# Kernel optimization log

Measured on AMD Instinct MI355X. Metric: run time of the kernel, lower is better.

## Reference

```python
import jax, jax.numpy as jnp
import numpy as np

B, S, WP = 64, 128, 18          # batch, words/sentence, padded chars/word
K = 3                            # char window size (module constant)
E = 128                          # embedding_dim
H = 256                          # hidden_dim
L = 4                            # cnn out channels (l=4 in module)
V = 50000                        # vocab size
A = 100                          # alphabet size
T = 50                           # tagset size


def setup_inputs() -> dict:
    key = jax.random.key(0)
    ks = jax.random.split(key, 14)
    n = lambda k, *sh: jax.random.normal(k, sh, dtype=jnp.float32) * 0.1
    return {
        "char_ids": jax.random.randint(ks[0], (B, S, WP), 0, A),
        "word_ids": jax.random.randint(ks[1], (B, S), 0, V),
        "char_emb": n(ks[2], A, E),
        "word_emb": n(ks[3], V + 1, E),
        "cnn_w": n(ks[4], L, K * E),
        "cnn_b": n(ks[5], L),
        "wih_f": n(ks[6], 4 * H, E),
        "whh_f": n(ks[7], 4 * H, H),
        "b_f": n(ks[8], 4 * H),
        "wih_b": n(ks[9], 4 * H, E),
        "whh_b": n(ks[10], 4 * H, H),
        "b_b": n(ks[11], 4 * H),
        "out_w": n(ks[12], T, 2 * H),
        "out_b": n(ks[13], T),
    }


def _lstm(x, Wih, Whh, b, reverse):
    # x: [S, B, E] -> hs: [S, B, H]; PyTorch gate order i, f, g, o
    hdim = Whh.shape[1]

    def step(carry, xt):
        h, c = carry
        z = xt @ Wih.T + h @ Whh.T + b
        i, f, g, o = jnp.split(z, 4, axis=-1)
        c = jax.nn.sigmoid(f) * c + jax.nn.sigmoid(i) * jnp.tanh(g)
        h = jax.nn.sigmoid(o) * jnp.tanh(c)
        return (h, c), h

    h0 = jnp.zeros((x.shape[1], hdim), x.dtype)
    _, hs = jax.lax.scan(step, (h0, h0), x, reverse=reverse)
    return hs


def reference(char_ids, word_ids, char_emb, word_emb, cnn_w, cnn_b,
              wih_f, whh_f, b_f, wih_b, whh_b, b_b, out_w, out_b):
    # --- per-word char CNN + max-pool (fully batched over B, S, positions) ---
    ce = char_emb[char_ids]                        # [B, S, WP, E]
    W = WP - (K - 1)                               # window positions per word
    windows = jnp.concatenate([ce[:, :, i:i + W] for i in range(K)], axis=-1)  # [B,S,W,K*E]
    phi = jnp.einsum('bswd,cd->bswc', windows, cnn_w) + cnn_b                  # [B,S,W,L]
    char_reprs = phi.max(axis=2)                   # [B, S, L] (unused by tag path, as in original)

    # --- word embeddings -> BiLSTM -> linear -> log_softmax over seq dim ---
    we = word_emb[word_ids]                        # [B, S, E]
    x = we.transpose(1, 0, 2)                      # [S, B, E]
    hf = _lstm(x, wih_f, whh_f, b_f, reverse=False)
    hb = _lstm(x, wih_b, whh_b, b_b, reverse=True)
    lstm_out = jnp.concatenate([hf, hb], axis=-1).transpose(1, 0, 2)  # [B, S, 2H]
    tag_space = lstm_out @ out_w.T + out_b         # [B, S, T]
    tag_scores = jax.nn.log_softmax(tag_space, axis=1)  # dim=1 as in original
    return tag_scores, char_reprs
```

## Files before the change

### kernel.cpp

```cpp
#include <hip/hip_runtime.h>
#include <hip/hip_bf16.h>

#define B_  64
#define S_  128
#define WP_ 18
#define K_  3
#define E_  128
#define H_  256
#define L_  4
#define T_  50

typedef __hip_bfloat16 bf16;

__device__ __forceinline__ float b2f(bf16 x) { return __bfloat162float(x); }
__device__ __forceinline__ bf16  f2b(float x) { return __float2bfloat16(x); }

__device__ __forceinline__ float fast_sigmoid(float x) {
    return 1.f / (1.f + __expf(-x));
}
__device__ __forceinline__ float fast_tanh(float x) {
    float a = fminf(fmaxf(2.f * x, -30.f), 30.f);
    float e = __expf(a);
    return (e - 1.f) / (e + 1.f);
}
__device__ __forceinline__ unsigned int pack2(float lo, float hi) {
    bf16 l = f2b(lo), h = f2b(hi);
    unsigned short ls = *(unsigned short*)&l, hs = *(unsigned short*)&h;
    return ((unsigned int)hs << 16) | ls;
}

#define DOT2(z, w, h) asm("v_dot2_f32_bf16 %0, %1, %2, %0" : "+v"(z) : "v"(w), "v"(h))
#define PIN4(V_) asm volatile("" : "+v"((V_).x), "+v"((V_).y), "+v"((V_).z), "+v"((V_).w))

__global__ void k_prep(const float* __restrict__ whh_f, const float* __restrict__ whh_b,
                       const float* __restrict__ wih_f, const float* __restrict__ wih_b,
                       unsigned int* __restrict__ wp_f, unsigned int* __restrict__ wp_b,
                       unsigned int* __restrict__ wihT2_f, unsigned int* __restrict__ wihT2_b) {
    int blk = blockIdx.x, t = threadIdx.x;
    if (blk < 1024) {
        const float* src   = (blk < 512) ? whh_f : whh_b;
        unsigned int* dst  = (blk < 512) ? wp_f  : wp_b;
        int d = ((blk & 511) << 8) + t;
        int m = d >> 12, rem = d & 4095;
        int td = rem >> 2, epair = rem & 3, e = epair << 1;
        int i = td >> 2, p = td & 3, g = m >> 3, kk = m & 7;
        int col = (g << 8) + i;
        int k = (p << 6) + (kk << 3) + e;
        float2 sv = *(const float2*)(src + col * 256 + k);
        dst[d] = pack2(sv.x, sv.y);
    } else {
        int id = blk - 1024;
        const float* src  = (id < 256) ? wih_f   : wih_b;
        unsigned int* dst = (id < 256) ? wihT2_f : wihT2_b;
        int d = ((id & 255) << 8) + t;
        int kp = d >> 10, j = d & 1023;
        float2 sv = *(const float2*)(src + j * 128 + 2 * kp);
        dst[d] = pack2(sv.x, sv.y);
    }
}

__global__ void k_input_proj(const int* __restrict__ word_ids,
                             const float* __restrict__ word_emb,
                             const unsigned int* __restrict__ wihT2_f, const float* __restrict__ b_f,
                             const unsigned int* __restrict__ wihT2_b, const float* __restrict__ b_b,
                             bf16* __restrict__ igq_f, bf16* __restrict__ igq_b) {
    int dir = blockIdx.y;
    const unsigned int* wihT2 = dir ? wihT2_b : wihT2_f;
    const float* bb  = dir ? b_b   : b_f;
    bf16* igq        = dir ? igq_b : igq_f;
    __shared__ unsigned int x2[32][64];
    int t  = threadIdx.x;
    int r0 = blockIdx.x * 32;
    for (int u = t; u < 32 * 64; u += 512) {
        int rr = u >> 6, ep = u & 63;
        int r = r0 + rr;
        int s = r >> 6, b = r & 63;
        int wid = word_ids[b * S_ + s];
        float2 ev = *(const float2*)(word_emb + (size_t)wid * E_ + 2 * ep);
        x2[rr][ep] = pack2(ev.x, ev.y);
    }
    __syncthreads();
    int j = t & 255, jh = t >> 8;
    float acc[2][32];
    #pragma unroll
    for (int c2 = 0; c2 < 2; ++c2) {
        float bv = bb[j + (2 * jh + c2) * 256];
        #pragma unroll
        for (int rr = 0; rr < 32; ++rr) acc[c2][rr] = bv;
    }
    for (int kp = 0; kp < 64; ++kp) {
        unsigned int wv0 = wihT2[kp * 1024 + j + (2 * jh) * 256];
        unsigned int wv1 = wihT2[kp * 1024 + j + (2 * jh + 1) * 256];
        #pragma unroll
        for (int rr = 0; rr < 32; ++rr) {
            unsigned int xp = x2[rr][kp];
            DOT2(acc[0][rr], wv0, xp);
            DOT2(acc[1][rr], wv1, xp);
        }
    }
    #pragma unroll
    for (int rr = 0; rr < 32; ++rr)
        *(unsigned int*)(igq + (size_t)(r0 + rr) * 1024 + j * 4 + 2 * jh) =
            pack2(acc[0][rr], acc[1][rr]);
}

__global__ __launch_bounds__(1024, 4) void k_lstm_cnn(
        const bf16* __restrict__ igq_f, const bf16* __restrict__ igq_b,
        const uint4* __restrict__ wp_f, const uint4* __restrict__ wp_b,
        unsigned int* __restrict__ hfp, unsigned int* __restrict__ hbp,
        const int* __restrict__ char_ids, const float* __restrict__ char_emb,
        const float* __restrict__ cnn_w, const float* __restrict__ cnn_b,
        float* __restrict__ out_char) {
    __shared__ uint4 wlds[9216];
    __shared__ __align__(16) unsigned int hpbuf[2][160];

    int t = threadIdx.x;

    if (blockIdx.x < 128) {
        int b   = blockIdx.x & 63;
        int dir = blockIdx.x >> 6;
        const bf16* igq  = dir ? igq_b : igq_f;
        const uint4* wp  = dir ? wp_b  : wp_f;
        unsigned int* hs = dir ? hbp   : hfp;

        int i = t >> 2, p = t & 3;

        for (int u = t; u < 9216; u += 1024) wlds[u] = wp[23 * 1024 + u];
        if (t < 320) ((unsigned int*)hpbuf)[t] = 0;
        float c_reg = 0.f;

        uint4 wreg[23];
        #pragma unroll
        for (int m = 0; m < 23; ++m) {
            wreg[m] = wp[m * 1024 + t];
            PIN4(wreg[m]);
        }
        __syncthreads();

        int cur = 0;
        int s0 = dir ? (S_ - 1) : 0;
        uint2 igu = *(const uint2*)&igq[((size_t)s0 * B_ + b) * 1024 + i * 4];

        for (int step = 0; step < S_; ++step) {
            int s = dir ? (S_ - 1 - step) : step;

            float z0 = 0.f, z1 = 0.f, z2 = 0.f, z3 = 0.f;
            if (p == 0) {
                z0 = __uint_as_float(igu.x << 16);
                z1 = __uint_as_float(igu.x & 0xffff0000u);
                z2 = __uint_as_float(igu.y << 16);
                z3 = __uint_as_float(igu.y & 0xffff0000u);
            }
            const char* hpc = (const char*)hpbuf[cur];
            #pragma unroll
            for (int kk = 0; kk < 8; ++kk) {
                uint4 hv = *(const uint4*)(hpc + p * 144 + kk * 16);
                {   uint4 wv = wreg[kk];
                    DOT2(z0, wv.x, hv.x); DOT2(z0, wv.y, hv.y);
                    DOT2(z0, wv.z, hv.z); DOT2(z0, wv.w, hv.w); }
                {   uint4 wv = wreg[8 + kk];
                    DOT2(z1, wv.x, hv.x); DOT2(z1, wv.y, hv.y);
                    DOT2(z1, wv.z, hv.z); DOT2(z1, wv.w, hv.w); }
                {   uint4 wv = (kk < 7) ? wreg[16 + kk] : wlds[t];
                    DOT2(z2, wv.x, hv.x); DOT2(z2, wv.y, hv.y);
                    DOT2(z2, wv.z, hv.z); DOT2(z2, wv.w, hv.w); }
                {   uint4 wv = wlds[(1 + kk) * 1024 + t];
                    DOT2(z3, wv.x, hv.x); DOT2(z3, wv.y, hv.y);
                    DOT2(z3, wv.z, hv.z); DOT2(z3, wv.w, hv.w); }
            }
            if (step + 1 < S_) {
                int sn = dir ? (S_ - 2 - step) : (step + 1);
                igu = *(const uint2*)&igq[((size_t)sn * B_ + b) * 1024 + i * 4];
            }
            z0 += __shfl_xor(z0, 1); z0 += __shfl_xor(z0, 2);
            z1 += __shfl_xor(z1, 1); z1 += __shfl_xor(z1, 2);
            z2 += __shfl_xor(z2, 1); z2 += __shfl_xor(z2, 2);
            z3 += __shfl_xor(z3, 1); z3 += __shfl_xor(z3, 2);
            if (p == 0) {
                float si = fast_sigmoid(z0);
                float sf = fast_sigmoid(z1);
                float tg = fast_tanh(z2);
                float so = fast_sigmoid(z3);
                c_reg = sf * c_reg + si * tg;
                float hn = so * fast_tanh(c_reg);
                char* dstb = (char*)hpbuf[cur ^ 1] + (i >> 6) * 144 + ((i >> 1) & 31) * 4 + (i & 1) * 2;
                *(bf16*)dstb = f2b(hn);
            }
            __syncthreads();
            if (t < 128) {
                hs[((size_t)s * B_ + b) * 128 + t] =
                    hpbuf[cur ^ 1][(t >> 5) * 36 + (t & 31)];
            }
            cur ^= 1;
        }
    } else {
        unsigned int* pool_u = (unsigned int*)wlds;
        float*        pool_f = (float*)wlds;
        int blkc = blockIdx.x - 128;

        for (int u = t; u < 4 * 192; u += 1024) {
            int c = u / 192, pe = u % 192;
            pool_u[c * 196 + pe] = pack2(cnn_w[c * 384 + 2 * pe], cnn_w[c * 384 + 2 * pe + 1]);
        }
        if (t < 4) pool_f[784 + t] = cnn_b[t];
        __syncthreads();

        int wv = t >> 6, lane = t & 63;
        unsigned int* cew = pool_u + 800 + wv * 1224;
        int pos = lane >> 2, c = lane & 3;

        #pragma unroll 1
        for (int j = 0; j < 4; ++j) {
            int word = (blkc * 16 + wv) * 4 + j;
            const int* ids = char_ids + word * WP_;
            for (int row = 0; row < WP_; ++row) {
                float2 ev = *(const float2*)(char_emb + (size_t)ids[row] * 128 + 2 * lane);
                cew[row * 68 + lane] = pack2(ev.x, ev.y);
            }
            float acc = 0.f;
            #pragma unroll
            for (int i = 0; i < K_; ++i) {
                const uint4* cr = (const uint4*)(cew + (pos + i) * 68);
                const uint4* wr = (const uint4*)(pool_u + c * 196 + i * 64);
                #pragma unroll
                for (int q = 0; q < 16; ++q) {
                    uint4 cv = cr[q], wq = wr[q];
                    DOT2(acc, wq.x, cv.x); DOT2(acc, wq.y, cv.y);
                    DOT2(acc, wq.z, cv.z); DOT2(acc, wq.w, cv.w);
                }
            }
            acc += pool_f[784 + c];
            #pragma unroll
            for (int off = 4; off < 64; off <<= 1) acc = fmaxf(acc, __shfl_xor(acc, off));
            if (lane < L_) out_char[(size_t)word * L_ + lane] = acc;
        }
    }
}

__global__ __launch_bounds__(1024) void k_tag_linear(
        const unsigned int* __restrict__ hfp, const unsigned int* __restrict__ hbp,
        const float* __restrict__ out_w, const float* __restrict__ out_b,
        float* __restrict__ tag) {
    __shared__ unsigned int ow[50 * 257];
    __shared__ unsigned int hv[16][256];
    int bs0 = blockIdx.x * 16;
    int t = threadIdx.x;
    for (int u = t; u < 12800; u += 1024) {
        int tt = u >> 8, kp = u & 255;
        float2 wv = *(const float2*)(out_w + tt * 512 + 2 * kp);
        ow[tt * 257 + kp] = pack2(wv.x, wv.y);
    }
    for (int u = t; u < 16 * 256; u += 1024) {
        int w = u >> 8, q = u & 255;
        int bs = bs0 + w;
        int b = bs >> 7, s = bs & 127;
        const unsigned int* src = (q < 128) ? hfp : hbp;
        hv[w][q] = src[((size_t)s * B_ + b) * 128 + (q & 127)];
    }
    __syncthreads();
    int w = t >> 6, tt = t & 63;
    if (tt < T_) {
        int bs = bs0 + w;
        int b = bs >> 7, s = bs & 127;
        float acc = out_b[tt];
        const unsigned int* owr = &ow[tt * 257];
        const unsigned int* hvr = hv[w];
        #pragma unroll 8
        for (int kp = 0; kp < 256; ++kp) DOT2(acc, owr[kp], hvr[kp]);
        tag[((size_t)b * T_ + tt) * S_ + s] = acc;
    }
}

__global__ void k_log_softmax(const float* __restrict__ tag, float* __restrict__ out) {
    int wid  = (blockIdx.x * 256 + threadIdx.x) >> 6;
    int lane = threadIdx.x & 63;
    if (wid >= B_ * T_) return;
    int b = wid / T_, t = wid % T_;
    const float* row = tag + (size_t)wid * S_;
    float v0 = row[lane], v1 = row[lane + 64];
    float m = fmaxf(v0, v1);
    #pragma unroll
    for (int off = 32; off; off >>= 1) m = fmaxf(m, __shfl_xor(m, off));
    float e = expf(v0 - m) + expf(v1 - m);
    #pragma unroll
    for (int off = 32; off; off >>= 1) e += __shfl_xor(e, off);
    float lse = m + logf(e);
    out[((size_t)b * S_ + lane)      * T_ + t] = v0 - lse;
    out[((size_t)b * S_ + lane + 64) * T_ + t] = v1 - lse;
}

extern "C" void kernel_launch(void* const* d_in, const int* in_sizes, int n_in,
                              void* d_out, int out_size, void* d_ws, size_t ws_size,
                              hipStream_t stream) {
    const int*   char_ids = (const int*)d_in[0];
    const int*   word_ids = (const int*)d_in[1];
    const float* char_emb = (const float*)d_in[2];
    const float* word_emb = (const float*)d_in[3];
    const float* cnn_w    = (const float*)d_in[4];
    const float* cnn_b    = (const float*)d_in[5];
    const float* wih_f    = (const float*)d_in[6];
    const float* whh_f    = (const float*)d_in[7];
    const float* b_f      = (const float*)d_in[8];
    const float* wih_b    = (const float*)d_in[9];
    const float* whh_b    = (const float*)d_in[10];
    const float* b_b      = (const float*)d_in[11];
    const float* out_w    = (const float*)d_in[12];
    const float* out_b    = (const float*)d_in[13];
    float* out = (float*)d_out;
    char* ws   = (char*)d_ws;

    size_t o = 0;
    unsigned int* wihT2_f = (unsigned int*)(ws + o); o += (size_t)64 * 1024 * 4;
    unsigned int* wihT2_b = (unsigned int*)(ws + o); o += (size_t)64 * 1024 * 4;
    unsigned int* wp_f    = (unsigned int*)(ws + o); o += (size_t)1024 * 128 * 4;
    unsigned int* wp_b    = (unsigned int*)(ws + o); o += (size_t)1024 * 128 * 4;
    bf16* igq_f  = (bf16*)(ws + o); o += (size_t)S_ * B_ * 1024 * 2;
    bf16* igq_b  = (bf16*)(ws + o); o += (size_t)S_ * B_ * 1024 * 2;
    unsigned int* hfp = (unsigned int*)(ws + o); o += (size_t)S_ * B_ * 128 * 4;
    unsigned int* hbp = (unsigned int*)(ws + o); o += (size_t)S_ * B_ * 128 * 4;
    float* tag   = (float*)(ws + o); o += (size_t)B_ * T_ * S_ * 4;

    k_prep<<<1536, 256, 0, stream>>>(whh_f, whh_b, wih_f, wih_b,
                                     wp_f, wp_b, wihT2_f, wihT2_b);
    k_input_proj<<<dim3(256, 2), 512, 0, stream>>>(word_ids, word_emb,
                                                   wihT2_f, b_f, wihT2_b, b_b, igq_f, igq_b);
    k_lstm_cnn<<<256, 1024, 0, stream>>>(igq_f, igq_b,
                                         (const uint4*)wp_f, (const uint4*)wp_b, hfp, hbp,
                                         char_ids, char_emb, cnn_w, cnn_b,
                                         out + (size_t)B_ * S_ * T_);
    k_tag_linear<<<B_ * S_ / 16, 1024, 0, stream>>>(hfp, hbp, out_w, out_b, tag);
    k_log_softmax<<<(B_ * T_ + 3) / 4, 256, 0, stream>>>(tag, out);
}
```

Measured before the change: 374.0 us.

## Halve LSTM block to 512 threads, two threads per hidden unit, more weights in registers

The recurrent LSTM block now uses 512 threads, each hidden unit split across 2 threads instead of 4. Each thread keeps 56 uint4 weight vectors in registers and reads only 8 from LDS. The weight packing in prep and the CNN word partition are reworked to match. The goal is to move more Whh reads from LDS into registers and shorten the cross-lane reduction, so each sequential step has less latency. In exchange each thread does twice the dot products and register pressure becomes very high, which risks spills.

```diff
diff --git a/kernel.cpp b/kernel.cpp
--- a/kernel.cpp
+++ b/kernel.cpp
@@ -41,11 +41,12 @@
         const float* src   = (blk < 512) ? whh_f : whh_b;
         unsigned int* dst  = (blk < 512) ? wp_f  : wp_b;
         int d = ((blk & 511) << 8) + t;
-        int m = d >> 12, rem = d & 4095;
-        int td = rem >> 2, epair = rem & 3, e = epair << 1;
-        int i = td >> 2, p = td & 3, g = m >> 3, kk = m & 7;
+        int m2 = d >> 11, rem = d & 2047;
+        int u = rem >> 2, e2 = rem & 3;
+        int i = u >> 1, p2 = u & 1;
+        int g = m2 >> 4, kk2 = m2 & 15;
         int col = (g << 8) + i;
-        int k = (p << 6) + (kk << 3) + e;
+        int k = (p2 << 7) + (kk2 << 3) + (e2 << 1);
         float2 sv = *(const float2*)(src + col * 256 + k);
         dst[d] = pack2(sv.x, sv.y);
     } else {
@@ -104,7 +105,7 @@
             pack2(acc[0][rr], acc[1][rr]);
 }
 
-__global__ __launch_bounds__(1024, 4) void k_lstm_cnn(
+__global__ __launch_bounds__(512, 2) void k_lstm_cnn(
         const bf16* __restrict__ igq_f, const bf16* __restrict__ igq_b,
         const uint4* __restrict__ wp_f, const uint4* __restrict__ wp_b,
         unsigned int* __restrict__ hfp, unsigned int* __restrict__ hbp,
@@ -123,16 +124,16 @@
         const uint4* wp  = dir ? wp_b  : wp_f;
         unsigned int* hs = dir ? hbp   : hfp;
 
-        int i = t >> 2, p = t & 3;
-
-        for (int u = t; u < 9216; u += 1024) wlds[u] = wp[23 * 1024 + u];
+        int i = t >> 1, p2 = t & 1;
+
+        for (int v = t; v < 4096; v += 512) wlds[v] = wp[56 * 512 + v];
         if (t < 320) ((unsigned int*)hpbuf)[t] = 0;
         float c_reg = 0.f;
 
-        uint4 wreg[23];
+        uint4 wreg[56];
         #pragma unroll
-        for (int m = 0; m < 23; ++m) {
-            wreg[m] = wp[m * 1024 + t];
+        for (int m = 0; m < 56; ++m) {
+            wreg[m] = wp[m * 512 + t];
             PIN4(wreg[m]);
         }
         __syncthreads();
@@ -145,7 +146,7 @@
             int s = dir ? (S_ - 1 - step) : step;
 
             float z0 = 0.f, z1 = 0.f, z2 = 0.f, z3 = 0.f;
-            if (p == 0) {
+            if (p2 == 0) {
                 z0 = __uint_as_float(igu.x << 16);
                 z1 = __uint_as_float(igu.x & 0xffff0000u);
                 z2 = __uint_as_float(igu.y << 16);
@@ -153,18 +154,18 @@
             }
             const char* hpc = (const char*)hpbuf[cur];
             #pragma unroll
-            for (int kk = 0; kk < 8; ++kk) {
-                uint4 hv = *(const uint4*)(hpc + p * 144 + kk * 16);
+            for (int kk = 0; kk < 16; ++kk) {
+                uint4 hv = *(const uint4*)(hpc + (p2 * 2 + (kk >> 3)) * 144 + (kk & 7) * 16);
                 {   uint4 wv = wreg[kk];
                     DOT2(z0, wv.x, hv.x); DOT2(z0, wv.y, hv.y);
                     DOT2(z0, wv.z, hv.z); DOT2(z0, wv.w, hv.w); }
-                {   uint4 wv = wreg[8 + kk];
+                {   uint4 wv = wreg[16 + kk];
                     DOT2(z1, wv.x, hv.x); DOT2(z1, wv.y, hv.y);
                     DOT2(z1, wv.z, hv.z); DOT2(z1, wv.w, hv.w); }
-                {   uint4 wv = (kk < 7) ? wreg[16 + kk] : wlds[t];
+                {   uint4 wv = wreg[32 + kk];
                     DOT2(z2, wv.x, hv.x); DOT2(z2, wv.y, hv.y);
                     DOT2(z2, wv.z, hv.z); DOT2(z2, wv.w, hv.w); }
-                {   uint4 wv = wlds[(1 + kk) * 1024 + t];
+                {   uint4 wv = (kk < 8) ? wreg[48 + kk] : wlds[(kk - 8) * 512 + t];
                     DOT2(z3, wv.x, hv.x); DOT2(z3, wv.y, hv.y);
                     DOT2(z3, wv.z, hv.z); DOT2(z3, wv.w, hv.w); }
             }
@@ -172,11 +173,11 @@
                 int sn = dir ? (S_ - 2 - step) : (step + 1);
                 igu = *(const uint2*)&igq[((size_t)sn * B_ + b) * 1024 + i * 4];
             }
-            z0 += __shfl_xor(z0, 1); z0 += __shfl_xor(z0, 2);
-            z1 += __shfl_xor(z1, 1); z1 += __shfl_xor(z1, 2);
-            z2 += __shfl_xor(z2, 1); z2 += __shfl_xor(z2, 2);
-            z3 += __shfl_xor(z3, 1); z3 += __shfl_xor(z3, 2);
-            if (p == 0) {
+            z0 += __shfl_xor(z0, 1);
+            z1 += __shfl_xor(z1, 1);
+            z2 += __shfl_xor(z2, 1);
+            z3 += __shfl_xor(z3, 1);
+            if (p2 == 0) {
                 float si = fast_sigmoid(z0);
                 float sf = fast_sigmoid(z1);
                 float tg = fast_tanh(z2);
@@ -198,7 +199,7 @@
         float*        pool_f = (float*)wlds;
         int blkc = blockIdx.x - 128;
 
-        for (int u = t; u < 4 * 192; u += 1024) {
+        for (int u = t; u < 4 * 192; u += 512) {
             int c = u / 192, pe = u % 192;
             pool_u[c * 196 + pe] = pack2(cnn_w[c * 384 + 2 * pe], cnn_w[c * 384 + 2 * pe + 1]);
         }
@@ -210,8 +211,8 @@
         int pos = lane >> 2, c = lane & 3;
 
         #pragma unroll 1
-        for (int j = 0; j < 4; ++j) {
-            int word = (blkc * 16 + wv) * 4 + j;
+        for (int j = 0; j < 8; ++j) {
+            int word = (blkc * 8 + wv) * 8 + j;
             const int* ids = char_ids + word * WP_;
             for (int row = 0; row < WP_; ++row) {
                 float2 ev = *(const float2*)(char_emb + (size_t)ids[row] * 128 + 2 * lane);
@@ -324,10 +325,10 @@
                                      wp_f, wp_b, wihT2_f, wihT2_b);
     k_input_proj<<<dim3(256, 2), 512, 0, stream>>>(word_ids, word_emb,
                                                    wihT2_f, b_f, wihT2_b, b_b, igq_f, igq_b);
-    k_lstm_cnn<<<256, 1024, 0, stream>>>(igq_f, igq_b,
-                                         (const uint4*)wp_f, (const uint4*)wp_b, hfp, hbp,
-                                         char_ids, char_emb, cnn_w, cnn_b,
-                                         out + (size_t)B_ * S_ * T_);
+    k_lstm_cnn<<<256, 512, 0, stream>>>(igq_f, igq_b,
+                                        (const uint4*)wp_f, (const uint4*)wp_b, hfp, hbp,
+                                        char_ids, char_emb, cnn_w, cnn_b,
+                                        out + (size_t)B_ * S_ * T_);
     k_tag_linear<<<B_ * S_ / 16, 1024, 0, stream>>>(hfp, hbp, out_w, out_b, tag);
     k_log_softmax<<<(B_ * T_ + 3) / 4, 256, 0, stream>>>(tag, out);
 }
```

Result: faster. 333.8 us, median of 2 (-10.8%).
